# Performance work log

Measured on AMD Instinct MI355X. Metric: run time of the kernel, lower is better.

The kernel has to match this reference:

```python
import jax, jax.numpy as jnp
import numpy as np

N = 100000       # nodes
E = 1600000      # edges (before self loops)
D = 128          # emb_dim
L = 5            # num_layer
NBOND = 62       # num_bond_type
NNODE = 2159     # num_node_type + 2
BN_EPS = 1e-5


def setup_inputs() -> dict:
    key = jax.random.key(0)
    ks = jax.random.split(key, 8)
    x = jax.random.randint(ks[0], (N, 1), 0, NNODE)
    edge_index = jax.random.randint(ks[1], (2, E), 0, N)
    edge_attr = jax.random.randint(ks[2], (E, 1), 0, NBOND)
    x_emb = jax.random.normal(ks[3], (NNODE, D), dtype=jnp.float32) * 0.02
    lin_w = jax.random.normal(ks[4], (L, D, D), dtype=jnp.float32) * (1.0 / np.sqrt(D))
    lin_b = jnp.zeros((L, D), jnp.float32)
    edge_tab = jax.random.normal(ks[5], (L, NBOND, D), dtype=jnp.float32) * 0.02
    bn_gamma = jnp.ones((L, D), jnp.float32)
    bn_beta = jnp.zeros((L, D), jnp.float32)
    return {"x": x, "edge_index": edge_index, "edge_attr": edge_attr,
            "x_emb": x_emb, "lin_w": lin_w, "lin_b": lin_b,
            "edge_tab": edge_tab, "bn_gamma": bn_gamma, "bn_beta": bn_beta}


def reference(x, edge_index, edge_attr, x_emb, lin_w, lin_b, edge_tab, bn_gamma, bn_beta):
    # node embedding lookup: x_embedding(x[:, 0])
    h = x_emb[x[:, 0]]                                  # [N, D]

    # add self loops (same for every layer in the torch code)
    loop = jnp.arange(N)
    src = jnp.concatenate([edge_index[0], loop])        # [E+N] = j (source)
    dst = jnp.concatenate([edge_index[1], loop])        # [E+N] = i (target)
    eids = jnp.concatenate([edge_attr[:, 0], jnp.zeros((N,), edge_attr.dtype)])

    # GCN symmetric norm: deg from row (=src), deg_inv_sqrt[row]*deg_inv_sqrt[col]
    deg = jax.ops.segment_sum(jnp.ones(src.shape, h.dtype), src, num_segments=N)
    dinv = jnp.where(deg > 0, jax.lax.rsqrt(deg), jnp.zeros_like(deg))
    norm = (dinv[src] * dinv[dst])[:, None]             # [E+N, 1]

    for l in range(L):
        # linear transform of nodes
        hl = h @ lin_w[l].T + lin_b[l]                  # [N, D]
        # message: norm * (x_j + edge_embedding), gather from source nodes
        msg = norm * (hl[src] + edge_tab[l][eids])      # [E+N, D]
        # aggr='add': scatter_add into target nodes
        agg = jax.ops.segment_sum(msg, dst, num_segments=N)  # [N, D]
        # BatchNorm1d (training-mode batch statistics, biased variance)
        mean = agg.mean(axis=0)
        var = jnp.mean((agg - mean) ** 2, axis=0)
        h = (agg - mean) * jax.lax.rsqrt(var + BN_EPS) * bn_gamma[l] + bn_beta[l]
        if l < L - 1:
            h = jax.nn.relu(h)
        # dropout with drop_ratio=0 is identity
    # JK == 'last'
    return h
```

## Files before the change

kernel.cpp:

```cpp
#include <hip/hip_runtime.h>

#define NN 100000
#define NE 1600000
#define NT (NE + NN)
#define DD 128
#define NL 5
#define NB 62
#define BN_EPS 1e-5f
#define NBUCK 391
#define PSUMNB 6250
#define RED1 128

typedef unsigned short ushort_t;
typedef unsigned int uint_t;
typedef short bf8 __attribute__((ext_vector_type(8)));
typedef float f32x4 __attribute__((ext_vector_type(4)));

static __device__ __forceinline__ float4 ld4(const float* p) { return *(const float4*)p; }

static __device__ __forceinline__ float bfhi(uint_t u) {
    uint_t x = u & 0xFFFF0000u;
    return __builtin_bit_cast(float, x);
}
static __device__ __forceinline__ float bflo(uint_t u) {
    uint_t x = u << 16;
    return __builtin_bit_cast(float, x);
}
static __device__ __forceinline__ ushort_t f2bf(float f) {
    uint_t u = __builtin_bit_cast(uint_t, f);
    u += 0x7FFFu + ((u >> 16) & 1u);
    return (ushort_t)(u >> 16);
}

static __device__ __forceinline__ void accum8(float* acc, uint4 hv, uint4 ev, float nr) {
    acc[0] = fmaf(nr, bflo(hv.x) + bflo(ev.x), acc[0]);
    acc[1] = fmaf(nr, bfhi(hv.x) + bfhi(ev.x), acc[1]);
    acc[2] = fmaf(nr, bflo(hv.y) + bflo(ev.y), acc[2]);
    acc[3] = fmaf(nr, bfhi(hv.y) + bfhi(ev.y), acc[3]);
    acc[4] = fmaf(nr, bflo(hv.z) + bflo(ev.z), acc[4]);
    acc[5] = fmaf(nr, bfhi(hv.z) + bfhi(ev.z), acc[5]);
    acc[6] = fmaf(nr, bflo(hv.w) + bflo(ev.w), acc[6]);
    acc[7] = fmaf(nr, bfhi(hv.w) + bfhi(ev.w), acc[7]);
}


__global__ void k_init(int* gbh_d, int* gbh_s, float* scale, float* shift,
                       int* row_ptr) {
    int i = blockIdx.x * 256 + threadIdx.x;
    if (i < NBUCK) { gbh_d[i] = 0; gbh_s[i] = 0; }
    if (i < DD) { scale[i] = 1.f; shift[i] = 0.f; }
    if (i == 0) row_ptr[NN] = NT;
}

__global__ void k_cvt(const float* __restrict__ src, ushort_t* __restrict__ dst,
                      int total) {
    int i = blockIdx.x * 256 + threadIdx.x;
    if (i < total) dst[i] = f2bf(src[i]);
}

__global__ __launch_bounds__(256) void k_binhist(const int* __restrict__ ei,
                                                 int* __restrict__ gbh_d,
                                                 int* __restrict__ gbh_s) {
    __shared__ int hd[NBUCK], hs[NBUCK];
    int tid = threadIdx.x;
    for (int b = tid; b < NBUCK; b += 256) { hd[b] = 0; hs[b] = 0; }
    __syncthreads();
    for (int idx = blockIdx.x * 256 + tid; idx < NT; idx += gridDim.x * 256) {
        int d = (idx < NE) ? ei[NE + idx] : idx - NE;
        atomicAdd(&hd[d >> 8], 1);
        if (idx < NE) atomicAdd(&hs[ei[idx] >> 8], 1);
    }
    __syncthreads();
    for (int b = tid; b < NBUCK; b += 256) {
        if (hd[b]) atomicAdd(&gbh_d[b], hd[b]);
        if (hs[b]) atomicAdd(&gbh_s[b], hs[b]);
    }
}

__global__ void k_scan391(const int* __restrict__ gbh_d, const int* __restrict__ gbh_s,
                          int* __restrict__ bb_d, int* __restrict__ cur_d,
                          int* __restrict__ bb_s, int* __restrict__ cur_s) {
    __shared__ int s[512];
    const int* g = blockIdx.x ? gbh_s : gbh_d;
    int* bb = blockIdx.x ? bb_s : bb_d;
    int* cur = blockIdx.x ? cur_s : cur_d;
    int t = threadIdx.x;
    int v = (t < NBUCK) ? g[t] : 0;
    s[t] = v;
    __syncthreads();
    for (int off = 1; off < 512; off <<= 1) {
        int val = (t >= off) ? s[t - off] : 0;
        __syncthreads();
        s[t] += val;
        __syncthreads();
    }
    if (t < NBUCK) { int e = s[t] - v; bb[t] = e; cur[t] = e; }
    if (t == 511) bb[NBUCK] = s[511];
}

#define CHUNK 4096
__global__ __launch_bounds__(256) void k_scat2(const int* __restrict__ ei,
                                               const int* __restrict__ ea,
                                               int* __restrict__ cur_d,
                                               int* __restrict__ cur_s,
                                               uint_t* __restrict__ rec_d,
                                               int* __restrict__ rec_s) {
    __shared__ int lhd[NBUCK], lbd[NBUCK], lhs[NBUCK], lbs[NBUCK];
    int tid = threadIdx.x;
    for (int b = tid; b < NBUCK; b += 256) { lhd[b] = 0; lhs[b] = 0; }
    __syncthreads();
    int base = blockIdx.x * CHUNK;
    uint_t rd[16];
    int rs[16], bkd[16], bks[16];
#pragma unroll
    for (int k = 0; k < 16; ++k) {
        int idx = base + tid + k * 256;
        bkd[k] = -1; bks[k] = -1;
        if (idx < NT) {
            int s, d, eid;
            if (idx < NE) {
                s = ei[idx]; d = ei[NE + idx]; eid = ea[idx];
                bks[k] = s >> 8; rs[k] = s;
                atomicAdd(&lhs[bks[k]], 1);
            } else {
                s = d = idx - NE; eid = 0;
            }
            bkd[k] = d >> 8;
            rd[k] = (uint_t)s | ((uint_t)eid << 17) | ((uint_t)(d & 255) << 24);
            atomicAdd(&lhd[bkd[k]], 1);
        }
    }
    __syncthreads();
    for (int b = tid; b < NBUCK; b += 256) {
        if (lhd[b]) lbd[b] = atomicAdd(&cur_d[b], lhd[b]);
        if (lhs[b]) lbs[b] = atomicAdd(&cur_s[b], lhs[b]);
    }
    __syncthreads();
    for (int b = tid; b < NBUCK; b += 256) { lhd[b] = 0; lhs[b] = 0; }
    __syncthreads();
#pragma unroll
    for (int k = 0; k < 16; ++k) {
        if (bkd[k] >= 0) {
            int rk = atomicAdd(&lhd[bkd[k]], 1);
            rec_d[lbd[bkd[k]] + rk] = rd[k];
        }
        if (bks[k] >= 0) {
            int rk = atomicAdd(&lhs[bks[k]], 1);
            rec_s[lbs[bks[k]] + rk] = rs[k];
        }
    }
}

__global__ __launch_bounds__(256) void k_srcfin(const int* __restrict__ rec,
                                                const int* __restrict__ bb,
                                                float* __restrict__ dinv) {
    __shared__ int h[256];
    int tid = threadIdx.x;
    h[tid] = 0;
    __syncthreads();
    int lo = bb[blockIdx.x], hi = bb[blockIdx.x + 1];
    for (int i = lo + tid; i < hi; i += 256) atomicAdd(&h[rec[i] & 255], 1);
    __syncthreads();
    int v = blockIdx.x * 256 + tid;
    if (v < NN) dinv[v] = rsqrtf((float)(h[tid] + 1));
}

__global__ __launch_bounds__(256) void k_dstfin(const uint_t* __restrict__ rec,
                                                const int* __restrict__ bb,
                                                const float* __restrict__ dinv,
                                                int* __restrict__ row_ptr,
                                                int2* __restrict__ s_pn) {
    __shared__ int h[256], sc[256], rpE[256];
    int tid = threadIdx.x;
    h[tid] = 0;
    __syncthreads();
    int lo = bb[blockIdx.x], hi = bb[blockIdx.x + 1];
    for (int i = lo + tid; i < hi; i += 256) atomicAdd(&h[(rec[i] >> 24) & 255], 1);
    __syncthreads();
    sc[tid] = h[tid];
    __syncthreads();
    for (int off = 1; off < 256; off <<= 1) {
        int val = (tid >= off) ? sc[tid - off] : 0;
        __syncthreads();
        sc[tid] += val;
        __syncthreads();
    }
    rpE[tid] = sc[tid] - h[tid];
    int v = blockIdx.x * 256 + tid;
    if (v < NN) row_ptr[v] = lo + rpE[tid];
    h[tid] = 0;
    __syncthreads();
    for (int i = lo + tid; i < hi; i += 256) {
        uint_t u = rec[i];
        int dl = (u >> 24) & 255;
        int rk = atomicAdd(&h[dl], 1);
        int slot = lo + rpE[dl] + rk;
        int s = u & 0x1FFFF;
        int e = (u >> 17) & 0x3F;
        float nm = dinv[s] * dinv[(blockIdx.x << 8) + dl];
        s_pn[slot] = make_int2(s | (e << 20), __float_as_int(nm));
    }
}

__global__ void k_h0b(const int* __restrict__ x, const float* __restrict__ emb,
                      ushort_t* __restrict__ Xb, int n) {
    int v = blockIdx.x * 16 + (threadIdx.x >> 4);
    if (v >= n) return;
    int c8 = (threadIdx.x & 15) * 8;
    const float* src = &emb[x[v] * DD + c8];
    uint_t pk[4];
#pragma unroll
    for (int j = 0; j < 4; ++j)
        pk[j] = (uint_t)f2bf(src[2 * j]) | ((uint_t)f2bf(src[2 * j + 1]) << 16);
    *(uint4*)&Xb[(size_t)v * DD + c8] = make_uint4(pk[0], pk[1], pk[2], pk[3]);
}


static __device__ __forceinline__ bf8 bn8(uint4 v, float4 sc0, float4 sc1,
                                          float4 sh0, float4 sh1, int relu) {
    const uint_t* pv = (const uint_t*)&v;
    float f[8];
    f[0] = fmaf(bflo(pv[0]), sc0.x, sh0.x); f[1] = fmaf(bfhi(pv[0]), sc0.y, sh0.y);
    f[2] = fmaf(bflo(pv[1]), sc0.z, sh0.z); f[3] = fmaf(bfhi(pv[1]), sc0.w, sh0.w);
    f[4] = fmaf(bflo(pv[2]), sc1.x, sh1.x); f[5] = fmaf(bfhi(pv[2]), sc1.y, sh1.y);
    f[6] = fmaf(bflo(pv[3]), sc1.z, sh1.z); f[7] = fmaf(bfhi(pv[3]), sc1.w, sh1.w);
    if (relu) {
#pragma unroll
        for (int j = 0; j < 8; ++j) f[j] = fmaxf(f[j], 0.f);
    }
    uint_t pk[4];
#pragma unroll
    for (int j = 0; j < 4; ++j)
        pk[j] = (uint_t)f2bf(f[2 * j]) | ((uint_t)f2bf(f[2 * j + 1]) << 16);
    uint4 r = make_uint4(pk[0], pk[1], pk[2], pk[3]);
    return __builtin_bit_cast(bf8, r);
}

__global__ __launch_bounds__(256, 3) void k_gemm(const ushort_t* __restrict__ Xb,
                                                 const ushort_t* __restrict__ Wb,
                                                 const float* __restrict__ bias,
                                                 const float* __restrict__ scale,
                                                 const float* __restrict__ shift,
                                                 ushort_t* __restrict__ C,
                                                 int n, int relu) {
    const int tid = threadIdx.x;
    const int r0 = blockIdx.x * 128;
    const int w = tid >> 6;
    const int lane = tid & 63;
    const int lr = lane & 15;
    const int lg = lane >> 4;

    f32x4 acc[2][8];
#pragma unroll
    for (int rf = 0; rf < 2; ++rf)
#pragma unroll
        for (int cf = 0; cf < 8; ++cf)
#pragma unroll
            for (int r = 0; r < 4; ++r) acc[rf][cf][r] = 0.f;

#pragma unroll
    for (int ks = 0; ks < 4; ++ks) {
        const int kb = (ks * 4 + lg) * 8;
        float4 sc0 = ld4(&scale[kb]), sc1 = ld4(&scale[kb + 4]);
        float4 sh0 = ld4(&shift[kb]), sh1 = ld4(&shift[kb + 4]);

        int row0 = r0 + w * 32 + lr;
        int row1 = row0 + 16;
        uint4 va = make_uint4(0, 0, 0, 0), vb = make_uint4(0, 0, 0, 0);
        if (row0 < n) va = *(const uint4*)&Xb[(size_t)row0 * DD + kb];
        if (row1 < n) vb = *(const uint4*)&Xb[(size_t)row1 * DD + kb];
        bf8 a0 = bn8(va, sc0, sc1, sh0, sh1, relu);
        bf8 a1 = bn8(vb, sc0, sc1, sh0, sh1, relu);

#pragma unroll
        for (int cf = 0; cf < 8; ++cf) {
            int col = cf * 16 + lr;
            bf8 b = *(const bf8*)&Wb[(size_t)col * DD + kb];
            acc[0][cf] = __builtin_amdgcn_mfma_f32_16x16x32_bf16(a0, b, acc[0][cf], 0, 0, 0);
            acc[1][cf] = __builtin_amdgcn_mfma_f32_16x16x32_bf16(a1, b, acc[1][cf], 0, 0, 0);
        }
    }

#pragma unroll
    for (int cf = 0; cf < 8; ++cf) {
        int col = cf * 16 + lr;
        float bi = bias[col];
#pragma unroll
        for (int rf = 0; rf < 2; ++rf) {
#pragma unroll
            for (int r = 0; r < 4; ++r) {
                int grow = r0 + w * 32 + rf * 16 + lg * 4 + r;
                if (grow < n) C[(size_t)grow * DD + col] = f2bf(acc[rf][cf][r] + bi);
            }
        }
    }
}

__global__ __launch_bounds__(256) void k_agg(const ushort_t* __restrict__ hl,
                                             const ushort_t* __restrict__ etab,
                                             const int* __restrict__ row_ptr,
                                             const int2* __restrict__ s_pn,
                                             ushort_t* __restrict__ aggb,
                                             float* __restrict__ psumA,
                                             float* __restrict__ psumB, int n) {
    __shared__ float lsA[4][DD], lsB[4][DD];
    int tid = threadIdx.x;

    int v = blockIdx.x * 16 + (tid >> 4);
    int lane8 = (tid & 15) * 8;
    int p0 = row_ptr[v], p1 = row_ptr[v + 1];
    float acc[8];
#pragma unroll
    for (int j = 0; j < 8; ++j) acc[j] = 0.f;

    int p = p0;
    for (; p + 4 <= p1; p += 4) {
        int2 a0 = s_pn[p], a1 = s_pn[p + 1], a2 = s_pn[p + 2], a3 = s_pn[p + 3];
        uint4 h0 = *(const uint4*)&hl[(size_t)(a0.x & 0xFFFFF) * DD + lane8];
        uint4 h1 = *(const uint4*)&hl[(size_t)(a1.x & 0xFFFFF) * DD + lane8];
        uint4 h2 = *(const uint4*)&hl[(size_t)(a2.x & 0xFFFFF) * DD + lane8];
        uint4 h3 = *(const uint4*)&hl[(size_t)(a3.x & 0xFFFFF) * DD + lane8];
        uint4 e0 = *(const uint4*)&etab[(a0.x >> 20) * DD + lane8];
        uint4 e1 = *(const uint4*)&etab[(a1.x >> 20) * DD + lane8];
        uint4 e2 = *(const uint4*)&etab[(a2.x >> 20) * DD + lane8];
        uint4 e3 = *(const uint4*)&etab[(a3.x >> 20) * DD + lane8];
        accum8(acc, h0, e0, __int_as_float(a0.y));
        accum8(acc, h1, e1, __int_as_float(a1.y));
        accum8(acc, h2, e2, __int_as_float(a2.y));
        accum8(acc, h3, e3, __int_as_float(a3.y));
    }
    for (; p < p1; ++p) {
        int2 a = s_pn[p];
        uint4 hv = *(const uint4*)&hl[(size_t)(a.x & 0xFFFFF) * DD + lane8];
        uint4 ev = *(const uint4*)&etab[(a.x >> 20) * DD + lane8];
        accum8(acc, hv, ev, __int_as_float(a.y));
    }

    uint_t pk[4];
#pragma unroll
    for (int j = 0; j < 4; ++j)
        pk[j] = (uint_t)f2bf(acc[2 * j]) | ((uint_t)f2bf(acc[2 * j + 1]) << 16);
    *(uint4*)&aggb[(size_t)v * DD + lane8] = make_uint4(pk[0], pk[1], pk[2], pk[3]);

    float s0[8], s1[8];
#pragma unroll
    for (int j = 0; j < 8; ++j) { s0[j] = acc[j]; s1[j] = acc[j] * acc[j]; }
#pragma unroll
    for (int m = 16; m <= 32; m <<= 1) {
#pragma unroll
        for (int j = 0; j < 8; ++j) {
            s0[j] += __shfl_xor(s0[j], m);
            s1[j] += __shfl_xor(s1[j], m);
        }
    }
    int wv = tid >> 6;
    int lane = tid & 63;
    if (lane < 16) {
#pragma unroll
        for (int j = 0; j < 8; ++j) {
            lsA[wv][lane8 + j] = s0[j];
            lsB[wv][lane8 + j] = s1[j];
        }
    }
    __syncthreads();
    if (tid < DD) {
        psumA[(size_t)blockIdx.x * DD + tid] =
            lsA[0][tid] + lsA[1][tid] + lsA[2][tid] + lsA[3][tid];
        psumB[(size_t)blockIdx.x * DD + tid] =
            lsB[0][tid] + lsB[1][tid] + lsB[2][tid] + lsB[3][tid];
    }
}

__global__ __launch_bounds__(256) void k_bnred(const float* __restrict__ psumA,
                                               const float* __restrict__ psumB,
                                               float* __restrict__ partA,
                                               float* __restrict__ partB) {
    __shared__ float sa[2][DD], sb[2][DD];
    int d = threadIdx.x & 127;
    int half = threadIdx.x >> 7;
    float a = 0.f, b = 0.f;
    int iend = min(blockIdx.x * 49 + 49, PSUMNB);
    for (int i = blockIdx.x * 49 + half; i < iend; i += 2) {
        a += psumA[(size_t)i * DD + d];
        b += psumB[(size_t)i * DD + d];
    }
    sa[half][d] = a; sb[half][d] = b;
    __syncthreads();
    if (threadIdx.x < DD) {
        partA[blockIdx.x * DD + d] = sa[0][d] + sa[1][d];
        partB[blockIdx.x * DD + d] = sb[0][d] + sb[1][d];
    }
}

__global__ __launch_bounds__(256) void k_bnfin(const float* __restrict__ partA,
                                               const float* __restrict__ partB,
                                               const float* __restrict__ gamma,
                                               const float* __restrict__ beta,
                                               float* __restrict__ scale,
                                               float* __restrict__ shift, int n) {
    __shared__ float sa[2][DD], sb[2][DD];
    int d = threadIdx.x & 127;
    int half = threadIdx.x >> 7;
    float a = 0.f, b = 0.f;
    for (int i = half; i < RED1; i += 2) {
        a += partA[i * DD + d];
        b += partB[i * DD + d];
    }
    sa[half][d] = a; sb[half][d] = b;
    __syncthreads();
    if (threadIdx.x < DD) {
        float s = sa[0][d] + sa[1][d];
        float ss = sb[0][d] + sb[1][d];
        float mean = s / (float)n;
        float var = ss / (float)n - mean * mean;
        float sc = gamma[d] * rsqrtf(var + BN_EPS);
        scale[d] = sc;
        shift[d] = beta[d] - mean * sc;
    }
}

__global__ void k_bnapply(const ushort_t* __restrict__ Xb, float* __restrict__ out,
                          const float* __restrict__ scale,
                          const float* __restrict__ shift, int total8) {
    int i = blockIdx.x * blockDim.x + threadIdx.x;
    int stride = gridDim.x * blockDim.x;
    for (; i < total8; i += stride) {
        int c8 = (i & 15) * 8;
        uint4 v = *(const uint4*)&Xb[(size_t)i * 8];
        float4 sc0 = ld4(&scale[c8]), sc1 = ld4(&scale[c8 + 4]);
        float4 sh0 = ld4(&shift[c8]), sh1 = ld4(&shift[c8 + 4]);
        float4 o0, o1;
        o0.x = fmaf(bflo(v.x), sc0.x, sh0.x);
        o0.y = fmaf(bfhi(v.x), sc0.y, sh0.y);
        o0.z = fmaf(bflo(v.y), sc0.z, sh0.z);
        o0.w = fmaf(bfhi(v.y), sc0.w, sh0.w);
        o1.x = fmaf(bflo(v.z), sc1.x, sh1.x);
        o1.y = fmaf(bfhi(v.z), sc1.y, sh1.y);
        o1.z = fmaf(bflo(v.w), sc1.z, sh1.z);
        o1.w = fmaf(bfhi(v.w), sc1.w, sh1.w);
        *(float4*)&out[(size_t)i * 8] = o0;
        *(float4*)&out[(size_t)i * 8 + 4] = o1;
    }
}


extern "C" void kernel_launch(void* const* d_in, const int* in_sizes, int n_in,
                              void* d_out, int out_size, void* d_ws, size_t ws_size,
                              hipStream_t stream) {
    const int* x        = (const int*)d_in[0];
    const int* ei       = (const int*)d_in[1];
    const int* ea       = (const int*)d_in[2];
    const float* x_emb  = (const float*)d_in[3];
    const float* lin_w  = (const float*)d_in[4];
    const float* lin_b  = (const float*)d_in[5];
    const float* etab   = (const float*)d_in[6];
    const float* gamma  = (const float*)d_in[7];
    const float* beta   = (const float*)d_in[8];
    float* OUT = (float*)d_out;

    char* w = (char*)d_ws;
    size_t off = 0;
    auto alloc = [&](size_t bytes) -> void* {
        off = (off + 255) & ~(size_t)255;
        void* p = w + off;
        off += bytes;
        return p;
    };
    ushort_t* Xb     = (ushort_t*)alloc((size_t)NN * DD * 2);
    ushort_t* hl     = (ushort_t*)alloc((size_t)NN * DD * 2);
    ushort_t* etabb  = (ushort_t*)alloc((size_t)NL * NB * DD * 2);
    ushort_t* Wb     = (ushort_t*)alloc((size_t)NL * DD * DD * 2);
    uint_t* rec_d    = (uint_t*)alloc((size_t)NT * 4);
    int*    rec_s    = (int*)alloc((size_t)NE * 4);
    int2*  s_pn      = (int2*)alloc((size_t)NT * 8);
    int*   rowp      = (int*)alloc((size_t)(NN + 1) * 4);
    float* dinv      = (float*)alloc((size_t)NN * 4);
    int*   gbh_d     = (int*)alloc((size_t)NBUCK * 4);
    int*   gbh_s     = (int*)alloc((size_t)NBUCK * 4);
    int*   bb_d      = (int*)alloc((size_t)(NBUCK + 1) * 4);
    int*   bb_s      = (int*)alloc((size_t)(NBUCK + 1) * 4);
    int*   cur_d     = (int*)alloc((size_t)NBUCK * 4);
    int*   cur_s     = (int*)alloc((size_t)NBUCK * 4);
    float* psumA     = (float*)alloc((size_t)DD * PSUMNB * 4);
    float* psumB     = (float*)alloc((size_t)DD * PSUMNB * 4);
    float* partA     = (float*)alloc((size_t)DD * RED1 * 4);
    float* partB     = (float*)alloc((size_t)DD * RED1 * 4);
    float* scale     = (float*)alloc((size_t)DD * 4);
    float* shift     = (float*)alloc((size_t)DD * 4);

    const int etabTot = NL * NB * DD;
    const int wTot = NL * DD * DD;

    k_init<<<(NN + 255) / 256, 256, 0, stream>>>(gbh_d, gbh_s, scale, shift, rowp);
    k_cvt<<<(etabTot + 255) / 256, 256, 0, stream>>>(etab, etabb, etabTot);
    k_cvt<<<(wTot + 255) / 256, 256, 0, stream>>>(lin_w, Wb, wTot);
    k_binhist<<<256, 256, 0, stream>>>(ei, gbh_d, gbh_s);
    k_scan391<<<2, 512, 0, stream>>>(gbh_d, gbh_s, bb_d, cur_d, bb_s, cur_s);
    k_scat2<<<(NT + CHUNK - 1) / CHUNK, 256, 0, stream>>>(ei, ea, cur_d, cur_s,
                                                          rec_d, rec_s);
    k_srcfin<<<NBUCK, 256, 0, stream>>>(rec_s, bb_s, dinv);
    k_dstfin<<<NBUCK, 256, 0, stream>>>(rec_d, bb_d, dinv, rowp, s_pn);
    k_h0b<<<(NN + 15) / 16, 256, 0, stream>>>(x, x_emb, Xb, NN);

    for (int l = 0; l < NL; ++l) {
        k_gemm<<<(NN + 127) / 128, 256, 0, stream>>>(Xb, Wb + (size_t)l * DD * DD,
                                                     lin_b + (size_t)l * DD,
                                                     scale, shift, hl, NN, l > 0 ? 1 : 0);
        k_agg<<<PSUMNB, 256, 0, stream>>>(hl, etabb + (size_t)l * NB * DD,
                                          rowp, s_pn, Xb, psumA, psumB, NN);
        k_bnred<<<RED1, 256, 0, stream>>>(psumA, psumB, partA, partB);
        k_bnfin<<<1, 256, 0, stream>>>(partA, partB, gamma + (size_t)l * DD,
                                       beta + (size_t)l * DD, scale, shift, NN);
    }
    k_bnapply<<<(NN * DD / 8 + 255) / 256, 256, 0, stream>>>(Xb, OUT, scale, shift,
                                                             NN * DD / 8);
}
```

Measured before the change: 755.2 us.

## Split edge pack/norm arrays and transpose MFMA operands for vectorized GEMM stores

Splits the interleaved int2 edge record into separate packed-index and norm arrays, which changes the read pattern in the aggregation inner loop. In the GEMM it swaps the MFMA A/B operands so each lane holds four consecutive output columns of one row. That lets the epilogue write 8-byte packed bf16 stores with a float4 bias load instead of scattered 2-byte stores. The aggregation now issues two separate loads per edge where it used to issue one 8-byte load.

```diff
diff --git a/kernel.cpp b/kernel.cpp
--- a/kernel.cpp
+++ b/kernel.cpp
@@ -169,7 +169,8 @@
                                                 const int* __restrict__ bb,
                                                 const float* __restrict__ dinv,
                                                 int* __restrict__ row_ptr,
-                                                int2* __restrict__ s_pn) {
+                                                int* __restrict__ s_pack,
+                                                float* __restrict__ s_norm) {
     __shared__ int h[256], sc[256], rpE[256];
     int tid = threadIdx.x;
     h[tid] = 0;
@@ -197,8 +198,8 @@
         int slot = lo + rpE[dl] + rk;
         int s = u & 0x1FFFF;
         int e = (u >> 17) & 0x3F;
-        float nm = dinv[s] * dinv[(blockIdx.x << 8) + dl];
-        s_pn[slot] = make_int2(s | (e << 20), __float_as_int(nm));
+        s_pack[slot] = s | (e << 20);
+        s_norm[slot] = dinv[s] * dinv[(blockIdx.x << 8) + dl];
     }
 }
 
@@ -276,21 +277,24 @@
         for (int cf = 0; cf < 8; ++cf) {
             int col = cf * 16 + lr;
             bf8 b = *(const bf8*)&Wb[(size_t)col * DD + kb];
-            acc[0][cf] = __builtin_amdgcn_mfma_f32_16x16x32_bf16(a0, b, acc[0][cf], 0, 0, 0);
-            acc[1][cf] = __builtin_amdgcn_mfma_f32_16x16x32_bf16(a1, b, acc[1][cf], 0, 0, 0);
-        }
-    }
-
-#pragma unroll
-    for (int cf = 0; cf < 8; ++cf) {
-        int col = cf * 16 + lr;
-        float bi = bias[col];
-#pragma unroll
-        for (int rf = 0; rf < 2; ++rf) {
-#pragma unroll
-            for (int r = 0; r < 4; ++r) {
-                int grow = r0 + w * 32 + rf * 16 + lg * 4 + r;
-                if (grow < n) C[(size_t)grow * DD + col] = f2bf(acc[rf][cf][r] + bi);
+            acc[0][cf] = __builtin_amdgcn_mfma_f32_16x16x32_bf16(b, a0, acc[0][cf], 0, 0, 0);
+            acc[1][cf] = __builtin_amdgcn_mfma_f32_16x16x32_bf16(b, a1, acc[1][cf], 0, 0, 0);
+        }
+    }
+
+#pragma unroll
+    for (int rf = 0; rf < 2; ++rf) {
+        int grow = r0 + w * 32 + rf * 16 + lr;
+        if (grow < n) {
+#pragma unroll
+            for (int cf = 0; cf < 8; ++cf) {
+                int c0 = cf * 16 + lg * 4;
+                float4 bi = ld4(&bias[c0]);
+                uint_t lo = (uint_t)f2bf(acc[rf][cf][0] + bi.x) |
+                            ((uint_t)f2bf(acc[rf][cf][1] + bi.y) << 16);
+                uint_t hi = (uint_t)f2bf(acc[rf][cf][2] + bi.z) |
+                            ((uint_t)f2bf(acc[rf][cf][3] + bi.w) << 16);
+                *(uint2*)&C[(size_t)grow * DD + c0] = make_uint2(lo, hi);
             }
         }
     }
@@ -299,7 +303,8 @@
 __global__ __launch_bounds__(256) void k_agg(const ushort_t* __restrict__ hl,
                                              const ushort_t* __restrict__ etab,
                                              const int* __restrict__ row_ptr,
-                                             const int2* __restrict__ s_pn,
+                                             const int* __restrict__ s_pack,
+                                             const float* __restrict__ s_norm,
                                              ushort_t* __restrict__ aggb,
                                              float* __restrict__ psumA,
                                              float* __restrict__ psumB, int n) {
@@ -315,25 +320,27 @@
 
     int p = p0;
     for (; p + 4 <= p1; p += 4) {
-        int2 a0 = s_pn[p], a1 = s_pn[p + 1], a2 = s_pn[p + 2], a3 = s_pn[p + 3];
-        uint4 h0 = *(const uint4*)&hl[(size_t)(a0.x & 0xFFFFF) * DD + lane8];
-        uint4 h1 = *(const uint4*)&hl[(size_t)(a1.x & 0xFFFFF) * DD + lane8];
-        uint4 h2 = *(const uint4*)&hl[(size_t)(a2.x & 0xFFFFF) * DD + lane8];
-        uint4 h3 = *(const uint4*)&hl[(size_t)(a3.x & 0xFFFFF) * DD + lane8];
-        uint4 e0 = *(const uint4*)&etab[(a0.x >> 20) * DD + lane8];
-        uint4 e1 = *(const uint4*)&etab[(a1.x >> 20) * DD + lane8];
-        uint4 e2 = *(const uint4*)&etab[(a2.x >> 20) * DD + lane8];
-        uint4 e3 = *(const uint4*)&etab[(a3.x >> 20) * DD + lane8];
-        accum8(acc, h0, e0, __int_as_float(a0.y));
-        accum8(acc, h1, e1, __int_as_float(a1.y));
-        accum8(acc, h2, e2, __int_as_float(a2.y));
-        accum8(acc, h3, e3, __int_as_float(a3.y));
+        int c0 = s_pack[p], c1 = s_pack[p + 1], c2 = s_pack[p + 2], c3 = s_pack[p + 3];
+        float n0 = s_norm[p], n1 = s_norm[p + 1], n2 = s_norm[p + 2], n3 = s_norm[p + 3];
+        uint4 h0 = *(const uint4*)&hl[(size_t)(c0 & 0xFFFFF) * DD + lane8];
+        uint4 h1 = *(const uint4*)&hl[(size_t)(c1 & 0xFFFFF) * DD + lane8];
+        uint4 h2 = *(const uint4*)&hl[(size_t)(c2 & 0xFFFFF) * DD + lane8];
+        uint4 h3 = *(const uint4*)&hl[(size_t)(c3 & 0xFFFFF) * DD + lane8];
+        uint4 e0 = *(const uint4*)&etab[(c0 >> 20) * DD + lane8];
+        uint4 e1 = *(const uint4*)&etab[(c1 >> 20) * DD + lane8];
+        uint4 e2 = *(const uint4*)&etab[(c2 >> 20) * DD + lane8];
+        uint4 e3 = *(const uint4*)&etab[(c3 >> 20) * DD + lane8];
+        accum8(acc, h0, e0, n0);
+        accum8(acc, h1, e1, n1);
+        accum8(acc, h2, e2, n2);
+        accum8(acc, h3, e3, n3);
     }
     for (; p < p1; ++p) {
-        int2 a = s_pn[p];
-        uint4 hv = *(const uint4*)&hl[(size_t)(a.x & 0xFFFFF) * DD + lane8];
-        uint4 ev = *(const uint4*)&etab[(a.x >> 20) * DD + lane8];
-        accum8(acc, hv, ev, __int_as_float(a.y));
+        int c = s_pack[p];
+        float nr = s_norm[p];
+        uint4 hv = *(const uint4*)&hl[(size_t)(c & 0xFFFFF) * DD + lane8];
+        uint4 ev = *(const uint4*)&etab[(c >> 20) * DD + lane8];
+        accum8(acc, hv, ev, nr);
     }
 
     uint_t pk[4];
@@ -472,7 +479,8 @@
     ushort_t* Wb     = (ushort_t*)alloc((size_t)NL * DD * DD * 2);
     uint_t* rec_d    = (uint_t*)alloc((size_t)NT * 4);
     int*    rec_s    = (int*)alloc((size_t)NE * 4);
-    int2*  s_pn      = (int2*)alloc((size_t)NT * 8);
+    int*   s_pack    = (int*)alloc((size_t)NT * 4);
+    float* s_norm    = (float*)alloc((size_t)NT * 4);
     int*   rowp      = (int*)alloc((size_t)(NN + 1) * 4);
     float* dinv      = (float*)alloc((size_t)NN * 4);
     int*   gbh_d     = (int*)alloc((size_t)NBUCK * 4);
@@ -499,7 +507,7 @@
     k_scat2<<<(NT + CHUNK - 1) / CHUNK, 256, 0, stream>>>(ei, ea, cur_d, cur_s,
                                                           rec_d, rec_s);
     k_srcfin<<<NBUCK, 256, 0, stream>>>(rec_s, bb_s, dinv);
-    k_dstfin<<<NBUCK, 256, 0, stream>>>(rec_d, bb_d, dinv, rowp, s_pn);
+    k_dstfin<<<NBUCK, 256, 0, stream>>>(rec_d, bb_d, dinv, rowp, s_pack, s_norm);
     k_h0b<<<(NN + 15) / 16, 256, 0, stream>>>(x, x_emb, Xb, NN);
 
     for (int l = 0; l < NL; ++l) {
@@ -507,7 +515,7 @@
                                                      lin_b + (size_t)l * DD,
                                                      scale, shift, hl, NN, l > 0 ? 1 : 0);
         k_agg<<<PSUMNB, 256, 0, stream>>>(hl, etabb + (size_t)l * NB * DD,
-                                          rowp, s_pn, Xb, psumA, psumB, NN);
+                                          rowp, s_pack, s_norm, Xb, psumA, psumB, NN);
         k_bnred<<<RED1, 256, 0, stream>>>(psumA, psumB, partA, partB);
         k_bnfin<<<1, 256, 0, stream>>>(partA, partB, gamma + (size_t)l * DD,
                                        beta + (size_t)l * DD, scale, shift, NN);
```

New measurement: 754.5 us. Within noise of the previous version (-0.1%).
